# Kernel tuning notes

Measured on AMD Instinct MI355X. Metric: run time of the kernel, lower is better.

The kernel has to match this reference:

```python
import math
import jax, jax.numpy as jnp
import numpy as np

B, DIM, L = 2, 512, 2048
H = 16
HD = DIM // H  # 32
R = 32
K = 3
GAMMA = 1.0


def _conv1d(x, w, b=None):
    # x: [B, Cin, L], w: [Cout, Cin, K] -> [B, Cout, L_out] (VALID)
    out = jax.lax.conv_general_dilated(
        x, w, window_strides=(1,), padding='VALID',
        dimension_numbers=('NCH', 'OIH', 'NCH'))
    if b is not None:
        out = out + b[None, :, None]
    return out


def _sketch_p4(x, G1, G2):
    # x: [B, H, L, HD]; G1, G2: [HD, R]
    # p=4: half = (1/sqrt(r)) * (x@G1 * x@G2); return half*half
    half = (x @ G1) * (x @ G2) / math.sqrt(R)
    return half * half  # [B, H, L, R]


def setup_inputs() -> dict:
    key = jax.random.key(0)
    ks = jax.random.split(key, 12)
    x = jax.random.normal(ks[0], (B, DIM, L), dtype=jnp.float32)
    # conv / linear params (kaiming-ish scale)
    q_w = jax.random.normal(ks[1], (DIM, DIM, K), dtype=jnp.float32) / math.sqrt(DIM * K)
    q_b = jnp.zeros((DIM,), dtype=jnp.float32)
    k_w = jax.random.normal(ks[2], (DIM, DIM, K), dtype=jnp.float32) / math.sqrt(DIM * K)
    k_b = jnp.zeros((DIM,), dtype=jnp.float32)
    v_w = jax.random.normal(ks[3], (DIM, DIM, 1), dtype=jnp.float32) / math.sqrt(DIM)
    proj_w = jax.random.normal(ks[4], (DIM, DIM), dtype=jnp.float32) / math.sqrt(DIM)
    proj_b = jnp.zeros((DIM,), dtype=jnp.float32)
    # learnable scalars
    gamma_q = jnp.ones((1,), dtype=jnp.float32) * GAMMA
    beta_q = jnp.zeros((1,), dtype=jnp.float32)
    gamma_k = jnp.ones((1,), dtype=jnp.float32) * GAMMA
    beta_k = jnp.zeros((1,), dtype=jnp.float32)
    # sketch matrices, std = 1/sqrt(r)
    G1q = jax.random.normal(ks[5], (HD, R), dtype=jnp.float32) / math.sqrt(R)
    G2q = jax.random.normal(ks[6], (HD, R), dtype=jnp.float32) / math.sqrt(R)
    G1k = jax.random.normal(ks[7], (HD, R), dtype=jnp.float32) / math.sqrt(R)
    G2k = jax.random.normal(ks[8], (HD, R), dtype=jnp.float32) / math.sqrt(R)
    return dict(x=x, q_w=q_w, q_b=q_b, k_w=k_w, k_b=k_b, v_w=v_w,
                proj_w=proj_w, proj_b=proj_b,
                gamma_q=gamma_q, beta_q=beta_q, gamma_k=gamma_k, beta_k=beta_k,
                G1q=G1q, G2q=G2q, G1k=G1k, G2k=G2k)


def reference(x, q_w, q_b, k_w, k_b, v_w, proj_w, proj_b,
              gamma_q, beta_q, gamma_k, beta_k, G1q, G2q, G1k, G2k):
    batch, dim, length = x.shape
    # causal left pad by K-1
    x_pad = jnp.pad(x, ((0, 0), (0, 0), (K - 1, 0)))
    q = _conv1d(x_pad, q_w, q_b)   # [B, DIM, L]
    k = _conv1d(x_pad, k_w, k_b)   # [B, DIM, L]
    v = _conv1d(x, v_w)            # [B, DIM, L] (1x1 conv, no bias)

    def shape(t):
        # [B, DIM, L] -> [B, H, HD, L] -> [B, H, L, HD]
        return t.reshape(batch, H, HD, length).transpose(0, 1, 3, 2)

    q, k, v = shape(q), shape(k), shape(v)
    q = gamma_q * q + beta_q
    k = gamma_k * k + beta_k
    phi_q = _sketch_p4(q, G1q, G2q)  # [B, H, L, R]
    phi_k = _sketch_p4(k, G1k, G2k)  # [B, H, L, R]
    scores = jnp.einsum('bhlr,bhmr->bhlm', phi_q, phi_k)  # [B, H, L, L]
    attn = scores / (scores.sum(axis=-1, keepdims=True) + 1e-6)
    o = jnp.einsum('bhlm,bhmd->bhld', attn, v)  # [B, H, L, HD]
    # [B, H, L, HD] -> [B, H, HD, L] -> [B, DIM, L] -> [B, L, DIM]
    o = o.transpose(0, 1, 3, 2).reshape(batch, dim, length).transpose(0, 2, 1)
    return o @ proj_w.T + proj_b
```

## Files before the change

### kernel.cpp

```cpp
#include <hip/hip_runtime.h>
#include <hip/hip_bf16.h>

#define DIMC 512
#define LEN  2048
#define NH   16
#define HD   32
#define RR   32

typedef __bf16 bf8_t __attribute__((ext_vector_type(8)));
typedef float  f4_t  __attribute__((ext_vector_type(4)));

__device__ __forceinline__ void gload16(const void* g, void* l) {
    __builtin_amdgcn_global_load_lds(
        (const __attribute__((address_space(1))) unsigned int*)g,
        (__attribute__((address_space(3))) unsigned int*)l, 16, 0, 0);
}

__global__ __launch_bounds__(256) void prep_kernel(
    const float* __restrict__ x,
    const float* __restrict__ qw, const float* __restrict__ kw,
    const float* __restrict__ vw, const float* __restrict__ pw,
    __bf16* __restrict__ xTh, __bf16* __restrict__ xTl,
    __bf16* __restrict__ Wrh, __bf16* __restrict__ Wrl,
    __bf16* __restrict__ pwh, __bf16* __restrict__ pwl,
    float* __restrict__ Skv)
{
    const int bid = blockIdx.x;
    const int tid = threadIdx.x;
    if (bid < 512) {
        __shared__ float tile[64][65];
        const int lblk = bid & 31, cblk = (bid >> 5) & 7, b = bid >> 8;
        const int l0 = lblk * 64, c0 = cblk * 64;
        #pragma unroll
        for (int it = 0; it < 4; ++it) {
            int cl = (tid >> 4) + it * 16;
            int ll = (tid & 15) * 4;
            float4 v4 = *reinterpret_cast<const float4*>(
                x + ((size_t)b * DIMC + c0 + cl) * LEN + l0 + ll);
            tile[cl][ll+0] = v4.x; tile[cl][ll+1] = v4.y;
            tile[cl][ll+2] = v4.z; tile[cl][ll+3] = v4.w;
        }
        __syncthreads();
        const int l  = tid & 63;
        const int cs = (tid >> 6) * 16;
        size_t rowbase = ((size_t)b * 2050 + l0 + l + 2) * DIMC + c0;
        #pragma unroll
        for (int half = 0; half < 2; ++half) {
            int c = cs + half * 8;
            bf8_t hi, lo;
            #pragma unroll
            for (int e = 0; e < 8; ++e) {
                float f = tile[c + e][l];
                __bf16 h = (__bf16)f;
                hi[e] = h;
                lo[e] = (__bf16)(f - (float)h);
            }
            *reinterpret_cast<bf8_t*>(xTh + rowbase + c) = hi;
            *reinterpret_cast<bf8_t*>(xTl + rowbase + c) = lo;
        }
        if (lblk == 0 && cblk == 0) {
            size_t pb = (size_t)b * 2050 * DIMC;
            #pragma unroll
            for (int e = 0; e < 4; ++e) {
                int p = tid * 4 + e;
                xTh[pb + p] = (__bf16)0.f;
                xTl[pb + p] = (__bf16)0.f;
            }
        }
    } else if (bid < 9728) {
        int idx = (bid - 512) * 256 + tid;
        int m   = idx / 1536;
        int rem = idx - m * 1536;
        int kk  = rem >> 9;
        int ci  = rem & 511;
        float f;
        if (m < 512)       f = qw[((size_t)m * 512 + ci) * 3 + kk];
        else if (m < 1024) f = kw[((size_t)(m - 512) * 512 + ci) * 3 + kk];
        else               f = (kk == 2) ? vw[(size_t)(m - 1024) * 512 + ci] : 0.f;
        __bf16 h = (__bf16)f;
        Wrh[idx] = h;
        Wrl[idx] = (__bf16)(f - (float)h);
    } else if (bid < 10752) {
        int idx = (bid - 9728) * 256 + tid;
        float f = pw[idx];
        __bf16 h = (__bf16)f;
        pwh[idx] = h;
        pwl[idx] = (__bf16)(f - (float)h);
    } else {
        int idx = (bid - 10752) * 256 + tid;
        if (idx < 33792) Skv[idx] = 0.f;
    }
}

__global__ __launch_bounds__(256) void conv_sketch_kernel(
    const __bf16* __restrict__ xTh, const __bf16* __restrict__ xTl,
    const __bf16* __restrict__ Wrh, const __bf16* __restrict__ Wrl,
    const float* __restrict__ q_b, const float* __restrict__ k_b,
    const float* __restrict__ gamma_q, const float* __restrict__ beta_q,
    const float* __restrict__ gamma_k, const float* __restrict__ beta_k,
    const float* __restrict__ G1q, const float* __restrict__ G2q,
    const float* __restrict__ G1k, const float* __restrict__ G2k,
    float* __restrict__ phi_q, float* __restrict__ phi_k,
    float* __restrict__ v)
{
    __shared__ __align__(16) char smem[24576];
    __bf16* sAh = (__bf16*)(smem);
    __bf16* sAl = (__bf16*)(smem + 8192);
    __bf16* sBh = (__bf16*)(smem + 16384);
    __bf16* sBl = (__bf16*)(smem + 20480);

    const int b   = blockIdx.z;
    const int mg  = blockIdx.y * 128;
    const int n0  = blockIdx.x * 64;
    const int tid = threadIdx.x;
    const int wave = tid >> 6, lane = tid & 63;
    const int wm = wave >> 1, wn = wave & 1;
    const int lr = lane & 15, k8 = lane >> 4;
    const int sec = mg >> 9;
    const int kks = (sec == 2) ? 2 : 0;

    const __bf16* xh = xTh + (size_t)b * 2050 * DIMC;
    const __bf16* xl = xTl + (size_t)b * 2050 * DIMC;

    f4_t acc[4][2];
    #pragma unroll
    for (int i = 0; i < 4; ++i)
        #pragma unroll
        for (int j = 0; j < 2; ++j)
            #pragma unroll
            for (int e = 0; e < 4; ++e) acc[i][j][e] = 0.f;

    const int sr0 = tid >> 2;
    const int ss  = tid & 3;
    const int sk0 = ((ss ^ ((sr0 >> 1) & 3)) << 3);
    const int sr1 = sr0 + 64;
    const int sk1 = ((ss ^ ((sr1 >> 1) & 3)) << 3);

    for (int kk = kks; kk < 3; ++kk) {
        const __bf16* wAh = Wrh + (size_t)mg * 1536 + kk * 512;
        const __bf16* wAl = Wrl + (size_t)mg * 1536 + kk * 512;
        const __bf16* xbh = xh + (size_t)(n0 + kk) * DIMC;
        const __bf16* xbl = xl + (size_t)(n0 + kk) * DIMC;
        for (int k0 = 0; k0 < 512; k0 += 32) {
            gload16(wAh + (size_t)sr0 * 1536 + k0 + sk0, (char*)sAh + tid * 16);
            gload16(wAh + (size_t)sr1 * 1536 + k0 + sk1, (char*)sAh + (256 + tid) * 16);
            gload16(wAl + (size_t)sr0 * 1536 + k0 + sk0, (char*)sAl + tid * 16);
            gload16(wAl + (size_t)sr1 * 1536 + k0 + sk1, (char*)sAl + (256 + tid) * 16);
            gload16(xbh + (size_t)sr0 * DIMC + k0 + sk0, (char*)sBh + tid * 16);
            gload16(xbl + (size_t)sr0 * DIMC + k0 + sk0, (char*)sBl + tid * 16);
            __syncthreads();
            bf8_t ah[4], al[4], bh[2], bl[2];
            #pragma unroll
            for (int i = 0; i < 4; ++i) {
                int row = wm * 64 + i * 16 + lr;
                int off = row * 64 + ((k8 ^ ((row >> 1) & 3)) << 4);
                ah[i] = *(const bf8_t*)((const char*)sAh + off);
                al[i] = *(const bf8_t*)((const char*)sAl + off);
            }
            #pragma unroll
            for (int j = 0; j < 2; ++j) {
                int row = wn * 32 + j * 16 + lr;
                int off = row * 64 + ((k8 ^ ((row >> 1) & 3)) << 4);
                bh[j] = *(const bf8_t*)((const char*)sBh + off);
                bl[j] = *(const bf8_t*)((const char*)sBl + off);
            }
            #pragma unroll
            for (int i = 0; i < 4; ++i)
                #pragma unroll
                for (int j = 0; j < 2; ++j) {
                    acc[i][j] = __builtin_amdgcn_mfma_f32_16x16x32_bf16(ah[i], bh[j], acc[i][j], 0, 0, 0);
                    acc[i][j] = __builtin_amdgcn_mfma_f32_16x16x32_bf16(ah[i], bl[j], acc[i][j], 0, 0, 0);
                    acc[i][j] = __builtin_amdgcn_mfma_f32_16x16x32_bf16(al[i], bh[j], acc[i][j], 0, 0, 0);
                }
            __syncthreads();
        }
    }

    const int cob = mg & 511;
    if (sec == 2) {
        #pragma unroll
        for (int i = 0; i < 4; ++i)
            #pragma unroll
            for (int r = 0; r < 4; ++r) {
                int co = cob + wm * 64 + i * 16 + k8 * 4 + r;
                float* orow = v + ((size_t)b * DIMC + co) * LEN;
                #pragma unroll
                for (int j = 0; j < 2; ++j)
                    orow[n0 + wn * 32 + j * 16 + lr] = acc[i][j][r];
            }
        return;
    }

    const float* G1 = (sec == 0) ? G1q : G1k;
    const float* G2 = (sec == 0) ? G2q : G2k;
    const float* bp = (sec == 0) ? q_b : k_b;
    const float ga  = (sec == 0) ? gamma_q[0] : gamma_k[0];
    const float be  = (sec == 0) ? beta_q[0]  : beta_k[0];
    float* phi      = (sec == 0) ? phi_q : phi_k;

    const int r = lane & 31;
    float g1r[32], g2r[32];
    #pragma unroll
    for (int d = 0; d < 32; ++d) {
        g1r[d] = G1[d * 32 + r];
        g2r[d] = G2[d * 32 + r];
    }
    float* q_s = (float*)smem;
    const int hb = cob >> 5;
    const int hl = wave >> 1;
    const int lbase = (wave & 1) * 32 + (lane >> 5) * 16;

    #pragma unroll
    for (int p = 0; p < 2; ++p) {
        if (wm == p) {
            #pragma unroll
            for (int i = 0; i < 4; ++i)
                #pragma unroll
                for (int rr = 0; rr < 4; ++rr) {
                    int lrow = i * 16 + k8 * 4 + rr;
                    float bv = bp[cob + p * 64 + lrow];
                    #pragma unroll
                    for (int j = 0; j < 2; ++j)
                        q_s[lrow * 66 + wn * 32 + j * 16 + lr] =
                            ga * (acc[i][j][rr] + bv) + be;
                }
        }
        __syncthreads();
        const int h = hb + 2 * p + hl;
        for (int t = 0; t < 16; ++t) {
            int lloc = lbase + t;
            float a = 0.f, cc = 0.f;
            #pragma unroll
            for (int d = 0; d < 32; ++d) {
                float qv = q_s[(hl * 32 + d) * 66 + lloc];
                a  += qv * g1r[d];
                cc += qv * g2r[d];
            }
            float hh = a * cc * 0.17677669529663687f;
            phi[(((size_t)b * NH + h) * LEN + n0 + lloc) * RR + r] = hh * hh;
        }
        __syncthreads();
    }
}

__global__ __launch_bounds__(256) void skv_kernel(
    const float* __restrict__ phi_k, const float* __restrict__ v,
    float* __restrict__ Skv, float* __restrict__ sk)
{
    const int b = blockIdx.z, h = blockIdx.y;
    const int l0 = blockIdx.x * 256;
    const int tid = threadIdx.x;
    __shared__ float ps[64][RR];
    __shared__ float vs[64][HD + 1];
    const int r  = tid >> 3;
    const int d4 = (tid & 7) * 4;
    float acc[4] = {0.f, 0.f, 0.f, 0.f};
    float skacc = 0.f;
    const float* pk = phi_k + ((size_t)(b * NH + h) * LEN + l0) * RR;
    const float* vb = v + ((size_t)b * DIMC + h * HD) * LEN + l0;
    for (int c = 0; c < 4; ++c) {
        for (int i = tid; i < 64 * 32; i += 256) {
            ps[i >> 5][i & 31] = pk[c * 64 * 32 + i];
            int dd = i >> 6, lc = i & 63;
            vs[lc][dd] = vb[(size_t)dd * LEN + c * 64 + lc];
        }
        __syncthreads();
        #pragma unroll 8
        for (int lc = 0; lc < 64; ++lc) {
            float pv = ps[lc][r];
            skacc += pv;
            #pragma unroll
            for (int j = 0; j < 4; ++j) acc[j] += pv * vs[lc][d4 + j];
        }
        __syncthreads();
    }
    const size_t base = (size_t)(b * NH + h) * RR + r;
    float* Sp = Skv + base * HD + d4;
    #pragma unroll
    for (int j = 0; j < 4; ++j) atomicAdd(Sp + j, acc[j]);
    if ((tid & 7) == 0) atomicAdd(sk + base, skacc);
}

__global__ __launch_bounds__(256) void onorm_kernel(
    const float* __restrict__ phi_q, const float* __restrict__ Skv,
    const float* __restrict__ sk, __bf16* __restrict__ o_h, __bf16* __restrict__ o_l)
{
    __shared__ float Ss[RR][HD];
    __shared__ float sks[RR];
    __shared__ float ph[8][RR + 1];
    const int b = blockIdx.z, hh = blockIdx.y;
    const int l0 = blockIdx.x * 8;
    const int tid = threadIdx.x;
    const int bh = b * NH + hh;
    for (int i = tid; i < RR * HD; i += 256) Ss[i >> 5][i & 31] = Skv[(size_t)bh * RR * HD + i];
    if (tid < RR) sks[tid] = sk[(size_t)bh * RR + tid];
    {
        const int r = tid & 31, li = tid >> 5;
        ph[li][r] = phi_q[((size_t)bh * LEN + l0 + li) * RR + r];
    }
    __syncthreads();
    const int d = tid & 31, li = tid >> 5;
    float num = 0.f, den = 0.f;
    #pragma unroll
    for (int r = 0; r < RR; ++r) {
        float p = ph[li][r];
        num += p * Ss[r][d];
        den += p * sks[r];
    }
    float val = num / (den + 1e-6f);
    __bf16 hv = (__bf16)val;
    size_t oi = ((size_t)b * LEN + l0 + li) * DIMC + hh * HD + d;
    o_h[oi] = hv;
    o_l[oi] = (__bf16)(val - (float)hv);
}

__global__ __launch_bounds__(256) void proj_mfma_kernel(
    const __bf16* __restrict__ oh, const __bf16* __restrict__ ol,
    const __bf16* __restrict__ pwh, const __bf16* __restrict__ pwl,
    const float* __restrict__ pb, float* __restrict__ out)
{
    __shared__ __bf16 sAh[128 * 32], sAl[128 * 32], sBh[64 * 32], sBl[64 * 32];
    const int m0  = blockIdx.y * 128;
    const int n0  = blockIdx.x * 64;
    const int tid = threadIdx.x;
    const int wave = tid >> 6, lane = tid & 63;
    const int wm = wave >> 1, wn = wave & 1;
    const int lr = lane & 15, k8 = lane >> 4;

    f4_t acc[4][2];
    #pragma unroll
    for (int i = 0; i < 4; ++i)
        #pragma unroll
        for (int j = 0; j < 2; ++j)
            #pragma unroll
            for (int e = 0; e < 4; ++e) acc[i][j][e] = 0.f;

    const int sr0 = tid >> 2;
    const int ss  = tid & 3;
    const int sk0 = ((ss ^ ((sr0 >> 1) & 3)) << 3);
    const int sr1 = sr0 + 64;
    const int sk1 = ((ss ^ ((sr1 >> 1) & 3)) << 3);

    for (int k0 = 0; k0 < 512; k0 += 32) {
        gload16(oh + (size_t)(m0 + sr0) * DIMC + k0 + sk0, (char*)sAh + tid * 16);
        gload16(oh + (size_t)(m0 + sr1) * DIMC + k0 + sk1, (char*)sAh + (256 + tid) * 16);
        gload16(ol + (size_t)(m0 + sr0) * DIMC + k0 + sk0, (char*)sAl + tid * 16);
        gload16(ol + (size_t)(m0 + sr1) * DIMC + k0 + sk1, (char*)sAl + (256 + tid) * 16);
        gload16(pwh + (size_t)(n0 + sr0) * DIMC + k0 + sk0, (char*)sBh + tid * 16);
        gload16(pwl + (size_t)(n0 + sr0) * DIMC + k0 + sk0, (char*)sBl + tid * 16);
        __syncthreads();
        bf8_t ah[4], al[4], bh[2], bl[2];
        #pragma unroll
        for (int i = 0; i < 4; ++i) {
            int row = wm * 64 + i * 16 + lr;
            int off = row * 64 + ((k8 ^ ((row >> 1) & 3)) << 4);
            ah[i] = *(const bf8_t*)((const char*)sAh + off);
            al[i] = *(const bf8_t*)((const char*)sAl + off);
        }
        #pragma unroll
        for (int j = 0; j < 2; ++j) {
            int row = wn * 32 + j * 16 + lr;
            int off = row * 64 + ((k8 ^ ((row >> 1) & 3)) << 4);
            bh[j] = *(const bf8_t*)((const char*)sBh + off);
            bl[j] = *(const bf8_t*)((const char*)sBl + off);
        }
        #pragma unroll
        for (int i = 0; i < 4; ++i)
            #pragma unroll
            for (int j = 0; j < 2; ++j) {
                acc[i][j] = __builtin_amdgcn_mfma_f32_16x16x32_bf16(ah[i], bh[j], acc[i][j], 0, 0, 0);
                acc[i][j] = __builtin_amdgcn_mfma_f32_16x16x32_bf16(ah[i], bl[j], acc[i][j], 0, 0, 0);
                acc[i][j] = __builtin_amdgcn_mfma_f32_16x16x32_bf16(al[i], bh[j], acc[i][j], 0, 0, 0);
            }
        __syncthreads();
    }
    #pragma unroll
    for (int j = 0; j < 2; ++j) {
        int n = n0 + wn * 32 + j * 16 + lr;
        float bv = pb[n];
        #pragma unroll
        for (int i = 0; i < 4; ++i)
            #pragma unroll
            for (int r = 0; r < 4; ++r) {
                int m = m0 + wm * 64 + i * 16 + k8 * 4 + r;
                out[(size_t)m * DIMC + n] = acc[i][j][r] + bv;
            }
    }
}

extern "C" void kernel_launch(void* const* d_in, const int* in_sizes, int n_in,
                              void* d_out, int out_size, void* d_ws, size_t ws_size,
                              hipStream_t stream)
{
    const float* x       = (const float*)d_in[0];
    const float* q_w     = (const float*)d_in[1];
    const float* q_b     = (const float*)d_in[2];
    const float* k_w     = (const float*)d_in[3];
    const float* k_b     = (const float*)d_in[4];
    const float* v_w     = (const float*)d_in[5];
    const float* proj_w  = (const float*)d_in[6];
    const float* proj_b  = (const float*)d_in[7];
    const float* gamma_q = (const float*)d_in[8];
    const float* beta_q  = (const float*)d_in[9];
    const float* gamma_k = (const float*)d_in[10];
    const float* beta_k  = (const float*)d_in[11];
    const float* G1q     = (const float*)d_in[12];
    const float* G2q     = (const float*)d_in[13];
    const float* G1k     = (const float*)d_in[14];
    const float* G2k     = (const float*)d_in[15];

    char* W = (char*)d_ws;
    constexpr size_t VB   = (size_t)2 * DIMC * LEN * 4;
    constexpr size_t XT   = (size_t)2 * 2050 * DIMC * 2;
    constexpr size_t WR   = (size_t)1536 * 1536 * 2;
    constexpr size_t PW   = (size_t)DIMC * DIMC * 2;
    constexpr size_t PHI  = (size_t)2 * NH * LEN * RR * 4;

    float*  v    = (float*)(W);
    __bf16* xTh  = (__bf16*)(W + VB);
    __bf16* xTl  = (__bf16*)(W + VB + XT);
    __bf16* Wrh  = (__bf16*)(W + VB + 2 * XT);
    __bf16* Wrl  = (__bf16*)(W + VB + 2 * XT + WR);
    __bf16* pwh  = (__bf16*)(W + VB + 2 * XT + 2 * WR);
    __bf16* pwl  = (__bf16*)(W + VB + 2 * XT + 2 * WR + PW);
    float*  phi_q = (float*)(W + VB + 2 * XT + 2 * WR + 2 * PW);
    float*  phi_k = (float*)(W + VB + 2 * XT + 2 * WR + 2 * PW + PHI);
    float*  Skv  = (float*)(W + VB + 2 * XT + 2 * WR + 2 * PW + 2 * PHI);
    float*  sk   = Skv + (size_t)2 * NH * RR * HD;
    __bf16* o_h  = xTh;
    __bf16* o_l  = (__bf16*)(W + VB + XT);

    prep_kernel<<<10884, 256, 0, stream>>>(x, q_w, k_w, v_w, proj_w,
                                           xTh, xTl, Wrh, Wrl, pwh, pwl, Skv);

    conv_sketch_kernel<<<dim3(LEN / 64, 12, 2), 256, 0, stream>>>(
        xTh, xTl, Wrh, Wrl, q_b, k_b, gamma_q, beta_q, gamma_k, beta_k,
        G1q, G2q, G1k, G2k, phi_q, phi_k, v);

    skv_kernel<<<dim3(LEN / 256, NH, 2), 256, 0, stream>>>(phi_k, v, Skv, sk);

    onorm_kernel<<<dim3(LEN / 8, NH, 2), 256, 0, stream>>>(phi_q, Skv, sk, o_h, o_l);

    proj_mfma_kernel<<<dim3(DIMC / 64, (2 * LEN) / 128), 256, 0, stream>>>(
        o_h, o_l, pwh, pwl, proj_b, (float*)d_out);
}
```

Baseline: 261.4 us.

## Split conv from sketch and run the sketch projection on MFMA

The fused conv+sketch kernel is split in two. The conv kernel now writes fp32 q, k and v to global memory. A new sketch kernel applies gamma/beta, splits the values into bf16 hi/lo parts and computes both sketch projections with split-bf16 MFMAs. This replaces the per-lane scalar FMA loop and the LDS-staged epilogue. The skv kernel is regridded to one 64-row chunk per block for more parallelism. The onorm kernel now handles four heads and 32 rows per block so the Skv/sk loads are reused. The cost is an extra global round trip for q/k, and workspace buffers are aliased to hold phi.

```diff
diff --git a/kernel.cpp b/kernel.cpp
--- a/kernel.cpp
+++ b/kernel.cpp
@@ -20,9 +20,12 @@
     const float* __restrict__ x,
     const float* __restrict__ qw, const float* __restrict__ kw,
     const float* __restrict__ vw, const float* __restrict__ pw,
+    const float* __restrict__ G1q, const float* __restrict__ G2q,
+    const float* __restrict__ G1k, const float* __restrict__ G2k,
     __bf16* __restrict__ xTh, __bf16* __restrict__ xTl,
     __bf16* __restrict__ Wrh, __bf16* __restrict__ Wrl,
     __bf16* __restrict__ pwh, __bf16* __restrict__ pwl,
+    __bf16* __restrict__ GTh, __bf16* __restrict__ GTl,
     float* __restrict__ Skv)
 {
     const int bid = blockIdx.x;
@@ -86,29 +89,33 @@
         __bf16 h = (__bf16)f;
         pwh[idx] = h;
         pwl[idx] = (__bf16)(f - (float)h);
-    } else {
+    } else if (bid < 10884) {
         int idx = (bid - 10752) * 256 + tid;
         if (idx < 33792) Skv[idx] = 0.f;
-    }
-}
-
-__global__ __launch_bounds__(256) void conv_sketch_kernel(
+    } else {
+        #pragma unroll
+        for (int m = 0; m < 4; ++m) {
+            const float* g = (m == 0) ? G1q : (m == 1) ? G2q : (m == 2) ? G1k : G2k;
+            #pragma unroll
+            for (int e = 0; e < 4; ++e) {
+                int i = tid * 4 + e;
+                int r = i >> 5, d = i & 31;
+                float f = g[d * 32 + r];
+                __bf16 h = (__bf16)f;
+                GTh[m * 1024 + i] = h;
+                GTl[m * 1024 + i] = (__bf16)(f - (float)h);
+            }
+        }
+    }
+}
+
+__global__ __launch_bounds__(256) void conv_mfma_kernel(
     const __bf16* __restrict__ xTh, const __bf16* __restrict__ xTl,
     const __bf16* __restrict__ Wrh, const __bf16* __restrict__ Wrl,
     const float* __restrict__ q_b, const float* __restrict__ k_b,
-    const float* __restrict__ gamma_q, const float* __restrict__ beta_q,
-    const float* __restrict__ gamma_k, const float* __restrict__ beta_k,
-    const float* __restrict__ G1q, const float* __restrict__ G2q,
-    const float* __restrict__ G1k, const float* __restrict__ G2k,
-    float* __restrict__ phi_q, float* __restrict__ phi_k,
-    float* __restrict__ v)
-{
-    __shared__ __align__(16) char smem[24576];
-    __bf16* sAh = (__bf16*)(smem);
-    __bf16* sAl = (__bf16*)(smem + 8192);
-    __bf16* sBh = (__bf16*)(smem + 16384);
-    __bf16* sBl = (__bf16*)(smem + 20480);
-
+    float* __restrict__ q, float* __restrict__ k, float* __restrict__ v)
+{
+    __shared__ __bf16 sAh[128 * 32], sAl[128 * 32], sBh[64 * 32], sBl[64 * 32];
     const int b   = blockIdx.z;
     const int mg  = blockIdx.y * 128;
     const int n0  = blockIdx.x * 64;
@@ -175,72 +182,122 @@
             __syncthreads();
         }
     }
-
+    float* outp = (sec == 0) ? q : (sec == 1) ? k : v;
+    const float* bp = (sec == 0) ? q_b : (sec == 1) ? k_b : nullptr;
     const int cob = mg & 511;
-    if (sec == 2) {
-        #pragma unroll
-        for (int i = 0; i < 4; ++i)
-            #pragma unroll
-            for (int r = 0; r < 4; ++r) {
-                int co = cob + wm * 64 + i * 16 + k8 * 4 + r;
-                float* orow = v + ((size_t)b * DIMC + co) * LEN;
+    #pragma unroll
+    for (int i = 0; i < 4; ++i)
+        #pragma unroll
+        for (int r = 0; r < 4; ++r) {
+            int co = cob + wm * 64 + i * 16 + k8 * 4 + r;
+            float bv = bp ? bp[co] : 0.f;
+            float* orow = outp + ((size_t)b * DIMC + co) * LEN;
+            #pragma unroll
+            for (int j = 0; j < 2; ++j)
+                orow[n0 + wn * 32 + j * 16 + lr] = acc[i][j][r];
+            if (bp) {
                 #pragma unroll
                 for (int j = 0; j < 2; ++j)
-                    orow[n0 + wn * 32 + j * 16 + lr] = acc[i][j][r];
-            }
-        return;
-    }
-
-    const float* G1 = (sec == 0) ? G1q : G1k;
-    const float* G2 = (sec == 0) ? G2q : G2k;
-    const float* bp = (sec == 0) ? q_b : k_b;
-    const float ga  = (sec == 0) ? gamma_q[0] : gamma_k[0];
-    const float be  = (sec == 0) ? beta_q[0]  : beta_k[0];
-    float* phi      = (sec == 0) ? phi_q : phi_k;
-
-    const int r = lane & 31;
-    float g1r[32], g2r[32];
-    #pragma unroll
-    for (int d = 0; d < 32; ++d) {
-        g1r[d] = G1[d * 32 + r];
-        g2r[d] = G2[d * 32 + r];
-    }
-    float* q_s = (float*)smem;
-    const int hb = cob >> 5;
-    const int hl = wave >> 1;
-    const int lbase = (wave & 1) * 32 + (lane >> 5) * 16;
-
-    #pragma unroll
-    for (int p = 0; p < 2; ++p) {
-        if (wm == p) {
-            #pragma unroll
-            for (int i = 0; i < 4; ++i)
-                #pragma unroll
-                for (int rr = 0; rr < 4; ++rr) {
-                    int lrow = i * 16 + k8 * 4 + rr;
-                    float bv = bp[cob + p * 64 + lrow];
-                    #pragma unroll
-                    for (int j = 0; j < 2; ++j)
-                        q_s[lrow * 66 + wn * 32 + j * 16 + lr] =
-                            ga * (acc[i][j][rr] + bv) + be;
-                }
-        }
-        __syncthreads();
-        const int h = hb + 2 * p + hl;
-        for (int t = 0; t < 16; ++t) {
-            int lloc = lbase + t;
-            float a = 0.f, cc = 0.f;
-            #pragma unroll
-            for (int d = 0; d < 32; ++d) {
-                float qv = q_s[(hl * 32 + d) * 66 + lloc];
-                a  += qv * g1r[d];
-                cc += qv * g2r[d];
-            }
-            float hh = a * cc * 0.17677669529663687f;
-            phi[(((size_t)b * NH + h) * LEN + n0 + lloc) * RR + r] = hh * hh;
-        }
-        __syncthreads();
-    }
+                    orow[n0 + wn * 32 + j * 16 + lr] = acc[i][j][r] + bv;
+            }
+        }
+}
+
+__global__ __launch_bounds__(256) void sketch_mfma_kernel(
+    const float* __restrict__ q, const float* __restrict__ k,
+    const float* __restrict__ gamma_q, const float* __restrict__ beta_q,
+    const float* __restrict__ gamma_k, const float* __restrict__ beta_k,
+    const __bf16* __restrict__ GTh, const __bf16* __restrict__ GTl,
+    float* __restrict__ phi_q, float* __restrict__ phi_k)
+{
+    __shared__ __align__(16) __bf16 sBh[128 * 32];
+    __shared__ __align__(16) __bf16 sBl[128 * 32];
+    const int z = blockIdx.z;
+    const int b = z & 1, isk = z >> 1;
+    const int h0 = blockIdx.y * 2;
+    const int l0 = blockIdx.x * 64;
+    const int tid = threadIdx.x;
+    const int wave = tid >> 6, lane = tid & 63;
+    const int lr = lane & 15, k8 = lane >> 4;
+
+    const float* src = isk ? k : q;
+    float* phi = isk ? phi_k : phi_q;
+    const float ga = isk ? gamma_k[0] : gamma_q[0];
+    const float be = isk ? beta_k[0]  : beta_q[0];
+
+    #pragma unroll
+    for (int it = 0; it < 4; ++it) {
+        int f = it * 256 + tid;
+        int row = f >> 4;
+        int l4  = (f & 15) * 4;
+        float4 v4 = *reinterpret_cast<const float4*>(
+            src + ((size_t)b * DIMC + h0 * 32 + row) * LEN + l0 + l4);
+        int d = row & 31, hloc = row >> 5;
+        float vv[4] = {v4.x, v4.y, v4.z, v4.w};
+        #pragma unroll
+        for (int e = 0; e < 4; ++e) {
+            float qp = ga * vv[e] + be;
+            __bf16 hh = (__bf16)qp;
+            int col = hloc * 64 + l4 + e;
+            int off = col * 32 + (((d >> 3) ^ (col & 3)) << 3) + (d & 7);
+            sBh[off] = hh;
+            sBl[off] = (__bf16)(qp - (float)hh);
+        }
+    }
+    __syncthreads();
+
+    const int cw = wave * 32;
+    bf8_t bh[2], bl[2];
+    #pragma unroll
+    for (int nt = 0; nt < 2; ++nt) {
+        int col = cw + nt * 16 + lr;
+        int off = col * 32 + ((k8 ^ (col & 3)) << 3);
+        bh[nt] = *(const bf8_t*)(sBh + off);
+        bl[nt] = *(const bf8_t*)(sBl + off);
+    }
+
+    const int matb = isk * 2;
+    f4_t t1[2][2], t2[2][2];
+    #pragma unroll
+    for (int mt = 0; mt < 2; ++mt)
+        #pragma unroll
+        for (int nt = 0; nt < 2; ++nt)
+            #pragma unroll
+            for (int e = 0; e < 4; ++e) { t1[mt][nt][e] = 0.f; t2[mt][nt][e] = 0.f; }
+
+    #pragma unroll
+    for (int mt = 0; mt < 2; ++mt) {
+        int abase = matb * 1024 + (mt * 16 + lr) * 32 + k8 * 8;
+        bf8_t a1h = *(const bf8_t*)(GTh + abase);
+        bf8_t a1l = *(const bf8_t*)(GTl + abase);
+        bf8_t a2h = *(const bf8_t*)(GTh + abase + 1024);
+        bf8_t a2l = *(const bf8_t*)(GTl + abase + 1024);
+        #pragma unroll
+        for (int nt = 0; nt < 2; ++nt) {
+            t1[mt][nt] = __builtin_amdgcn_mfma_f32_16x16x32_bf16(a1h, bh[nt], t1[mt][nt], 0, 0, 0);
+            t1[mt][nt] = __builtin_amdgcn_mfma_f32_16x16x32_bf16(a1h, bl[nt], t1[mt][nt], 0, 0, 0);
+            t1[mt][nt] = __builtin_amdgcn_mfma_f32_16x16x32_bf16(a1l, bh[nt], t1[mt][nt], 0, 0, 0);
+            t2[mt][nt] = __builtin_amdgcn_mfma_f32_16x16x32_bf16(a2h, bh[nt], t2[mt][nt], 0, 0, 0);
+            t2[mt][nt] = __builtin_amdgcn_mfma_f32_16x16x32_bf16(a2h, bl[nt], t2[mt][nt], 0, 0, 0);
+            t2[mt][nt] = __builtin_amdgcn_mfma_f32_16x16x32_bf16(a2l, bh[nt], t2[mt][nt], 0, 0, 0);
+        }
+    }
+
+    #pragma unroll
+    for (int mt = 0; mt < 2; ++mt)
+        #pragma unroll
+        for (int nt = 0; nt < 2; ++nt) {
+            int col = cw + nt * 16 + lr;
+            int l = col & 63, hloc = col >> 6;
+            f4_t out;
+            #pragma unroll
+            for (int e = 0; e < 4; ++e) {
+                float hh = t1[mt][nt][e] * t2[mt][nt][e] * 0.17677669529663687f;
+                out[e] = hh * hh;
+            }
+            *reinterpret_cast<f4_t*>(phi +
+                (((size_t)b * NH + h0 + hloc) * LEN + l0 + l) * RR + mt * 16 + k8 * 4) = out;
+        }
 }
 
 __global__ __launch_bounds__(256) void skv_kernel(
@@ -248,7 +305,7 @@
     float* __restrict__ Skv, float* __restrict__ sk)
 {
     const int b = blockIdx.z, h = blockIdx.y;
-    const int l0 = blockIdx.x * 256;
+    const int l0 = blockIdx.x * 64;
     const int tid = threadIdx.x;
     __shared__ float ps[64][RR];
     __shared__ float vs[64][HD + 1];
@@ -258,21 +315,18 @@
     float skacc = 0.f;
     const float* pk = phi_k + ((size_t)(b * NH + h) * LEN + l0) * RR;
     const float* vb = v + ((size_t)b * DIMC + h * HD) * LEN + l0;
-    for (int c = 0; c < 4; ++c) {
-        for (int i = tid; i < 64 * 32; i += 256) {
-            ps[i >> 5][i & 31] = pk[c * 64 * 32 + i];
-            int dd = i >> 6, lc = i & 63;
-            vs[lc][dd] = vb[(size_t)dd * LEN + c * 64 + lc];
-        }
-        __syncthreads();
-        #pragma unroll 8
-        for (int lc = 0; lc < 64; ++lc) {
-            float pv = ps[lc][r];
-            skacc += pv;
-            #pragma unroll
-            for (int j = 0; j < 4; ++j) acc[j] += pv * vs[lc][d4 + j];
-        }
-        __syncthreads();
+    for (int i = tid; i < 64 * 32; i += 256) {
+        ps[i >> 5][i & 31] = pk[i];
+        int dd = i >> 6, lc = i & 63;
+        vs[lc][dd] = vb[(size_t)dd * LEN + lc];
+    }
+    __syncthreads();
+    #pragma unroll 8
+    for (int lc = 0; lc < 64; ++lc) {
+        float pv = ps[lc][r];
+        skacc += pv;
+        #pragma unroll
+        for (int j = 0; j < 4; ++j) acc[j] += pv * vs[lc][d4 + j];
     }
     const size_t base = (size_t)(b * NH + h) * RR + r;
     float* Sp = Skv + base * HD + d4;
@@ -285,33 +339,41 @@
     const float* __restrict__ phi_q, const float* __restrict__ Skv,
     const float* __restrict__ sk, __bf16* __restrict__ o_h, __bf16* __restrict__ o_l)
 {
-    __shared__ float Ss[RR][HD];
-    __shared__ float sks[RR];
-    __shared__ float ph[8][RR + 1];
-    const int b = blockIdx.z, hh = blockIdx.y;
-    const int l0 = blockIdx.x * 8;
+    __shared__ float Ss[4][RR][HD];
+    __shared__ float sks[4][RR];
+    __shared__ float ph[32][RR + 1];
+    const int b = blockIdx.z, hg = blockIdx.y;
+    const int l0 = blockIdx.x * 32;
     const int tid = threadIdx.x;
-    const int bh = b * NH + hh;
-    for (int i = tid; i < RR * HD; i += 256) Ss[i >> 5][i & 31] = Skv[(size_t)bh * RR * HD + i];
-    if (tid < RR) sks[tid] = sk[(size_t)bh * RR + tid];
-    {
-        const int r = tid & 31, li = tid >> 5;
-        ph[li][r] = phi_q[((size_t)bh * LEN + l0 + li) * RR + r];
-    }
-    __syncthreads();
-    const int d = tid & 31, li = tid >> 5;
-    float num = 0.f, den = 0.f;
-    #pragma unroll
-    for (int r = 0; r < RR; ++r) {
-        float p = ph[li][r];
-        num += p * Ss[r][d];
-        den += p * sks[r];
-    }
-    float val = num / (den + 1e-6f);
-    __bf16 hv = (__bf16)val;
-    size_t oi = ((size_t)b * LEN + l0 + li) * DIMC + hh * HD + d;
-    o_h[oi] = hv;
-    o_l[oi] = (__bf16)(val - (float)hv);
+    const int bh0 = b * NH + hg * 4;
+    for (int i = tid; i < 4096; i += 256) {
+        int hh = i >> 10;
+        Ss[hh][(i >> 5) & 31][i & 31] = Skv[(size_t)(bh0 + hh) * (RR * HD) + (i & 1023)];
+    }
+    if (tid < 128) sks[tid >> 5][tid & 31] = sk[(size_t)(bh0 + (tid >> 5)) * RR + (tid & 31)];
+    const int d = tid & 31, ls = tid >> 5;
+    for (int h = 0; h < 4; ++h) {
+        __syncthreads();
+        for (int i = tid; i < 1024; i += 256)
+            ph[i >> 5][i & 31] = phi_q[((size_t)(bh0 + h) * LEN + l0 + (i >> 5)) * RR + (i & 31)];
+        __syncthreads();
+        #pragma unroll
+        for (int lt = 0; lt < 4; ++lt) {
+            int l = lt * 8 + ls;
+            float num = 0.f, den = 0.f;
+            #pragma unroll
+            for (int r = 0; r < RR; ++r) {
+                float p = ph[l][r];
+                num += p * Ss[h][r][d];
+                den += p * sks[h][r];
+            }
+            float val = num / (den + 1e-6f);
+            __bf16 hv = (__bf16)val;
+            size_t oi = ((size_t)b * LEN + l0 + l) * DIMC + (hg * 4 + h) * HD + d;
+            o_h[oi] = hv;
+            o_l[oi] = (__bf16)(val - (float)hv);
+        }
+    }
 }
 
 __global__ __launch_bounds__(256) void proj_mfma_kernel(
@@ -410,36 +472,45 @@
     const float* G2k     = (const float*)d_in[15];
 
     char* W = (char*)d_ws;
-    constexpr size_t VB   = (size_t)2 * DIMC * LEN * 4;
+    constexpr size_t QKV  = (size_t)2 * DIMC * LEN * 4;
     constexpr size_t XT   = (size_t)2 * 2050 * DIMC * 2;
     constexpr size_t WR   = (size_t)1536 * 1536 * 2;
     constexpr size_t PW   = (size_t)DIMC * DIMC * 2;
-    constexpr size_t PHI  = (size_t)2 * NH * LEN * RR * 4;
-
-    float*  v    = (float*)(W);
-    __bf16* xTh  = (__bf16*)(W + VB);
-    __bf16* xTl  = (__bf16*)(W + VB + XT);
-    __bf16* Wrh  = (__bf16*)(W + VB + 2 * XT);
-    __bf16* Wrl  = (__bf16*)(W + VB + 2 * XT + WR);
-    __bf16* pwh  = (__bf16*)(W + VB + 2 * XT + 2 * WR);
-    __bf16* pwl  = (__bf16*)(W + VB + 2 * XT + 2 * WR + PW);
-    float*  phi_q = (float*)(W + VB + 2 * XT + 2 * WR + 2 * PW);
-    float*  phi_k = (float*)(W + VB + 2 * XT + 2 * WR + 2 * PW + PHI);
-    float*  Skv  = (float*)(W + VB + 2 * XT + 2 * WR + 2 * PW + 2 * PHI);
+    constexpr size_t GT   = (size_t)4 * 1024 * 2;
+
+    float*  q    = (float*)(W);
+    float*  k    = (float*)(W + QKV);
+    float*  v    = (float*)(W + 2 * QKV);
+    __bf16* xTh  = (__bf16*)(W + 3 * QKV);
+    __bf16* xTl  = (__bf16*)(W + 3 * QKV + XT);
+    __bf16* Wrh  = (__bf16*)(W + 3 * QKV + 2 * XT);
+    __bf16* Wrl  = (__bf16*)(W + 3 * QKV + 2 * XT + WR);
+    __bf16* pwh  = (__bf16*)(W + 3 * QKV + 2 * XT + 2 * WR);
+    __bf16* pwl  = (__bf16*)(W + 3 * QKV + 2 * XT + 2 * WR + PW);
+    __bf16* GTh  = (__bf16*)(W + 3 * QKV + 2 * XT + 2 * WR + 2 * PW);
+    __bf16* GTl  = (__bf16*)(W + 3 * QKV + 2 * XT + 2 * WR + 2 * PW + GT);
+    float*  Skv  = (float*)(W + 3 * QKV + 2 * XT + 2 * WR + 2 * PW + 2 * GT);
     float*  sk   = Skv + (size_t)2 * NH * RR * HD;
-    __bf16* o_h  = xTh;
-    __bf16* o_l  = (__bf16*)(W + VB + XT);
-
-    prep_kernel<<<10884, 256, 0, stream>>>(x, q_w, k_w, v_w, proj_w,
-                                           xTh, xTl, Wrh, Wrl, pwh, pwl, Skv);
-
-    conv_sketch_kernel<<<dim3(LEN / 64, 12, 2), 256, 0, stream>>>(
-        xTh, xTl, Wrh, Wrl, q_b, k_b, gamma_q, beta_q, gamma_k, beta_k,
-        G1q, G2q, G1k, G2k, phi_q, phi_k, v);
-
-    skv_kernel<<<dim3(LEN / 256, NH, 2), 256, 0, stream>>>(phi_k, v, Skv, sk);
-
-    onorm_kernel<<<dim3(LEN / 8, NH, 2), 256, 0, stream>>>(phi_q, Skv, sk, o_h, o_l);
+    float*  phi_q = (float*)xTh;
+    float*  phi_k = (float*)Wrh;
+    __bf16* o_h   = (__bf16*)q;
+    __bf16* o_l   = (__bf16*)(W + QKV / 2);
+
+    prep_kernel<<<10885, 256, 0, stream>>>(x, q_w, k_w, v_w, proj_w,
+                                           G1q, G2q, G1k, G2k,
+                                           xTh, xTl, Wrh, Wrl, pwh, pwl,
+                                           GTh, GTl, Skv);
+
+    conv_mfma_kernel<<<dim3(LEN / 64, 12, 2), 256, 0, stream>>>(
+        xTh, xTl, Wrh, Wrl, q_b, k_b, q, k, v);
+
+    sketch_mfma_kernel<<<dim3(LEN / 64, NH / 2, 4), 256, 0, stream>>>(
+        q, k, gamma_q, beta_q, gamma_k, beta_k, GTh, GTl, phi_q, phi_k);
+
+    skv_kernel<<<dim3(LEN / 64, NH, 2), 256, 0, stream>>>(phi_k, v, Skv, sk);
+
+    onorm_kernel<<<dim3(LEN / 32, NH / 4, 2), 256, 0, stream>>>(
+        phi_q, Skv, sk, o_h, o_l);
 
     proj_mfma_kernel<<<dim3(DIMC / 64, (2 * LEN) / 128), 256, 0, stream>>>(
         o_h, o_l, pwh, pwl, proj_b, (float*)d_out);
```

After: 229.0 us. 12.4% less time.
